# Optimization experiments

Hardware: AMD Instinct MI355X
Metric: run time of the kernel (lower is better)

Reference implementation:

```python
import jax, jax.numpy as jnp
import numpy as np

B, SQ, SK = 2, 2048, 2048   # batch, n_query, n_memory
D, H, DFF = 1024, 16, 1024  # model dim, heads, ffn dim (must equal D per source constraints)
DH = D // H                 # head dim = 64
NEG = 1e9


def _split_heads(x):
    # (B, S, D) -> (B, H, S, DH)
    b, s, _ = x.shape
    return x.reshape(b, s, H, DH).transpose(0, 2, 1, 3)


def setup_inputs() -> dict:
    key = jax.random.key(0)
    ks = jax.random.split(key, 10)
    s = 0.02
    return {
        "q": jax.random.normal(ks[0], (B, SQ, D), jnp.float32),
        "k": jax.random.normal(ks[1], (B, SK, D), jnp.float32),
        "v": jax.random.normal(ks[2], (B, SK, D), jnp.float32),
        "Win_w": jax.random.normal(ks[3], (DFF, D), jnp.float32) * s,
        "Win_b": jnp.zeros((DFF,), jnp.float32),
        "Wff_w": jax.random.normal(ks[4], (D, DFF), jnp.float32) * s,
        "Wff_b": jnp.zeros((D,), jnp.float32),
        "Wout_w": jax.random.normal(ks[5], (D, D), jnp.float32) * s,
        "Wout_b": jnp.zeros((D,), jnp.float32),
        "attn_mask": jax.random.randint(ks[6], (B, SK), 0, 2, jnp.int32),
    }


def reference(q, k, v, Win_w, Win_b, Wff_w, Wff_b, Wout_w, Wout_b, attn_mask):
    # projections (in_linear; k,v additionally pass through out_linear as in source)
    qh = q @ Win_w.T + Win_b
    kh = (k @ Win_w.T + Win_b) @ Wout_w.T + Wout_b
    vh = (v @ Win_w.T + Win_b) @ Wout_w.T + Wout_b
    qh = qh * (D ** -0.5)

    qh, kh, vh = _split_heads(qh), _split_heads(kh), _split_heads(vh)

    # additive mask bias: 0 where mask==1, -1e9 where mask==0, broadcast over heads/queries
    bias = (attn_mask.astype(jnp.float32) - 1.0) * NEG  # (B, SK)
    scores = jnp.einsum("bhqd,bhkd->bhqk", qh, kh) + bias[:, None, None, :]
    probs = jax.nn.softmax(scores, axis=-1)
    out = jnp.einsum("bhqk,bhkd->bhqd", probs, vh)

    # merge heads: (B, H, SQ, DH) -> (B, SQ, D)
    out = out.transpose(0, 2, 1, 3).reshape(B, SQ, D)

    out = out @ Wff_w.T + Wff_b
    out = out @ Wout_w.T + Wout_b
    return out
```

## Files before the change

### kernel.cpp

```cpp
#include <hip/hip_runtime.h>
#include <cstdint>
#include <cstddef>

using u16 = unsigned short;
using u32 = unsigned int;

typedef __attribute__((ext_vector_type(8))) short short8;
typedef __attribute__((ext_vector_type(4))) float f32x4;

#define MFMA16(a, b, c) __builtin_amdgcn_mfma_f32_16x16x32_bf16((a), (b), (c), 0, 0, 0)

#define QSCALE 0.0450842200f

__device__ __forceinline__ u16 f2bf(float f) {
  u32 u = __float_as_uint(f);
  return (u16)((u + 0x7FFFu + ((u >> 16) & 1u)) >> 16);
}

__device__ __forceinline__ u32 pack_bf16(float a, float b) {
  u32 r;
  asm("v_cvt_pk_bf16_f32 %0, %1, %2" : "=v"(r) : "v"(a), "v"(b));
  return r;
}

__device__ __forceinline__ void gload_lds16(const u16* g, u16* l) {
  __builtin_amdgcn_global_load_lds((const __attribute__((address_space(1))) void*)g,
                                   (__attribute__((address_space(3))) void*)l, 16, 0, 0);
}

__global__ __launch_bounds__(256) void prep_all(
    const float* __restrict__ q, const float* __restrict__ k, const float* __restrict__ v,
    const float* __restrict__ Wout_w, const float* __restrict__ Win_w,
    const float* __restrict__ Wff_w, const float* __restrict__ Win_b,
    const float* __restrict__ Wout_b, u16* __restrict__ X,
    u16* __restrict__ Woutb, u16* __restrict__ Winb,
    u16* __restrict__ WinT, u16* __restrict__ WffT,
    float* __restrict__ bias2, float* __restrict__ bias1f) {
  __shared__ float tile[64][68];
  const int t = threadIdx.x;
  const int bid = blockIdx.x;
  if (bid < 12288) {
    int i4 = bid * 256 + t;
    const float* src = (i4 < 1048576) ? q : (i4 < 2097152) ? k : v;
    int loc = i4 & 1048575;
    float4 w = reinterpret_cast<const float4*>(src)[loc];
    u32 lo = (u32)f2bf(w.x) | ((u32)f2bf(w.y) << 16);
    u32 hi = (u32)f2bf(w.z) | ((u32)f2bf(w.w) << 16);
    reinterpret_cast<uint2*>(X)[i4] = make_uint2(lo, hi);
  } else if (bid < 14336) {
    const int wb = bid - 12288;
    const float* src = wb < 1024 ? Wout_w : Win_w;
    u16* dst = wb < 1024 ? Woutb : Winb;
    const float sc = wb < 1024 ? 1.0f : QSCALE;
    int i = (wb & 1023) * 256 + t;
    float4 vv = reinterpret_cast<const float4*>(src)[i];
    u32 lo = (u32)f2bf(vv.x * sc) | ((u32)f2bf(vv.y * sc) << 16);
    u32 hi = (u32)f2bf(vv.z * sc) | ((u32)f2bf(vv.w * sc) << 16);
    reinterpret_cast<uint2*>(dst)[i] = make_uint2(lo, hi);
  } else if (bid < 14848) {
    const int tb = bid - 14336;
    const float* in = tb < 256 ? Win_w : Wff_w;
    u16* out = tb < 256 ? WinT : WffT;
    const int tix = tb & 255;
    const int bx = (tix >> 4) * 64, by = (tix & 15) * 64;
    const int r = t >> 2, c16 = (t & 3) * 16;
#pragma unroll
    for (int i = 0; i < 4; ++i)
      *reinterpret_cast<float4*>(&tile[r][c16 + i * 4]) =
          *reinterpret_cast<const float4*>(&in[(size_t)(bx + r) * 1024 + by + c16 + i * 4]);
    __syncthreads();
    const int jj = t >> 2, i16 = (t & 3) * 16;
#pragma unroll
    for (int i = 0; i < 4; ++i) {
      uint2 p;
      p.x = (u32)f2bf(tile[i16 + i * 4 + 0][jj]) | ((u32)f2bf(tile[i16 + i * 4 + 1][jj]) << 16);
      p.y = (u32)f2bf(tile[i16 + i * 4 + 2][jj]) | ((u32)f2bf(tile[i16 + i * 4 + 3][jj]) << 16);
      *reinterpret_cast<uint2*>(&out[(size_t)(by + jj) * 1024 + bx + i16 + i * 4]) = p;
    }
  } else if (bid < 15104) {
    const int w = t >> 6, l = t & 63;
    const int j = (bid - 14848) * 4 + w;
    const float4* Wr = reinterpret_cast<const float4*>(Wout_w + (size_t)j * 1024);
    const float4* br = reinterpret_cast<const float4*>(Win_b);
    float s = 0.f;
    for (int i = l; i < 256; i += 64) {
      float4 a = Wr[i], b = br[i];
      s += a.x * b.x + a.y * b.y + a.z * b.z + a.w * b.w;
    }
#pragma unroll
    for (int o = 1; o < 64; o <<= 1) s += __shfl_xor(s, o);
    if (l == 0) bias2[j] = s + Wout_b[j];
  } else {
    float4 vv = reinterpret_cast<const float4*>(Win_b)[t];
    vv.x *= QSCALE; vv.y *= QSCALE; vv.z *= QSCALE; vv.w *= QSCALE;
    reinterpret_cast<float4*>(bias1f)[t] = vv;
  }
}

__global__ __launch_bounds__(256) void gemm_w2(const u16* __restrict__ A,
                                               const u16* __restrict__ Bt0,
                                               const u16* __restrict__ Bt1,
                                               u16* __restrict__ C0,
                                               u16* __restrict__ C1) {
  const int bid = blockIdx.x;
  const int xcd = bid & 7, local = bid >> 3;
  const int z = local >> 5;
  const int mt = xcd * 2 + ((local >> 4) & 1);
  const int nt = local & 15;
  const u16* Bt = z ? Bt1 : Bt0;
  u16* C = z ? C1 : C0;
  __shared__ __align__(16) u16 As[2][4096];
  __shared__ __align__(16) u16 Bs[2][4096];
  const int t = threadIdx.x, w = t >> 6, l = t & 63;
  const int l15 = l & 15, l4 = l >> 4;
  const int m0 = mt * 64, n0 = nt * 64;
  f32x4 acc[4] = {};
  const int row0 = t >> 3, cs0 = t & 7;
  const int c0 = cs0 ^ (row0 & 7);
  const int row1 = row0 + 32;
  const int c1 = cs0 ^ (row1 & 7);
  const u16* gA0 = A + (size_t)(m0 + row0) * 1024 + c0 * 8;
  const u16* gA1 = A + (size_t)(m0 + row1) * 1024 + c1 * 8;
  const u16* gB0 = Bt + (size_t)(n0 + row0) * 1024 + c0 * 8;
  const u16* gB1 = Bt + (size_t)(n0 + row1) * 1024 + c1 * 8;
#define W2_STAGE(KK, DST)                             \
  gload_lds16(gA0 + (KK), &As[DST][0] + w * 512);     \
  gload_lds16(gA1 + (KK), &As[DST][2048] + w * 512);  \
  gload_lds16(gB0 + (KK), &Bs[DST][0] + w * 512);     \
  gload_lds16(gB1 + (KK), &Bs[DST][2048] + w * 512);
  W2_STAGE(0, 0)
  for (int step = 0; step < 16; ++step) {
    const int c = step & 1;
    __syncthreads();
    if (step < 15) { W2_STAGE((step + 1) * 64, c ^ 1) }
#pragma unroll
    for (int ks = 0; ks < 2; ++ks) {
      const int cc = ks * 4 + l4;
      short8 bfr = *reinterpret_cast<const short8*>(&Bs[c][(w * 16 + l15) * 64 + ((cc ^ (l15 & 7)) * 8)]);
#pragma unroll
      for (int i = 0; i < 4; ++i) {
        short8 afr = *reinterpret_cast<const short8*>(&As[c][(i * 16 + l15) * 64 + ((cc ^ (l15 & 7)) * 8)]);
        acc[i] = MFMA16(afr, bfr, acc[i]);
      }
    }
  }
#pragma unroll
  for (int i = 0; i < 4; ++i)
#pragma unroll
    for (int j = 0; j < 4; ++j)
      C[(size_t)(m0 + i * 16 + l4 * 4 + j) * 1024 + n0 + w * 16 + l15] = f2bf(acc[i][j]);
}

__global__ __launch_bounds__(256) void proj(const u16* __restrict__ X,
                                            const u16* __restrict__ Winb,
                                            const u16* __restrict__ Wc2,
                                            const float* __restrict__ bias1f,
                                            const float* __restrict__ bias2,
                                            u16* __restrict__ Qh,
                                            u16* __restrict__ Kp,
                                            u16* __restrict__ VT) {
  __shared__ __align__(16) u16 As[2][4096];
  __shared__ __align__(16) u16 Bs[2][4096];
  const int t = threadIdx.x, w = t >> 6, l = t & 63;
  const int l15 = l & 15, l4 = l >> 4;
  const int bid = blockIdx.x;
  const int xcd = bid & 7, local = bid >> 3;
  const int mt = xcd * 12 + (local >> 3);
  const int nt = local & 7;
  const int seg = mt >> 5;
  const int m0 = mt * 128;
  const int n0 = nt * 128;
  const int wr = (w >> 1) * 64, wc = (w & 1) * 64;
  const u16* Bt = seg == 0 ? Winb : Wc2;
  const float* bias = seg == 0 ? bias1f : bias2;

  f32x4 acc[4][4] = {};
  const int srow = t >> 2;
  const int sck = (t & 3) ^ ((t >> 3) & 3);
  const u16* gA = X + (size_t)(m0 + srow) * 1024 + sck * 8;
  const u16* gB = Bt + (size_t)(n0 + srow) * 1024 + sck * 8;
#define PJ_STAGE(KK, DST)                                   \
  gload_lds16(gA + (KK), &As[DST][0] + w * 512);            \
  gload_lds16(gA + (KK) + 65536, &As[DST][2048] + w * 512); \
  gload_lds16(gB + (KK), &Bs[DST][0] + w * 512);            \
  gload_lds16(gB + (KK) + 65536, &Bs[DST][2048] + w * 512);
  PJ_STAGE(0, 0)
  const int sw = (l15 >> 1) & 3;
  for (int step = 0; step < 32; ++step) {
    const int c = step & 1;
    __syncthreads();
    if (step < 31) { PJ_STAGE((step + 1) * 32, c ^ 1) }
    short8 af[4], bf[4];
#pragma unroll
    for (int i = 0; i < 4; ++i)
      af[i] = *reinterpret_cast<const short8*>(&As[c][(wr + i * 16 + l15) * 32 + ((l4 ^ sw) * 8)]);
#pragma unroll
    for (int i = 0; i < 4; ++i)
      bf[i] = *reinterpret_cast<const short8*>(&Bs[c][(wc + i * 16 + l15) * 32 + ((l4 ^ sw) * 8)]);
#pragma unroll
    for (int mi = 0; mi < 4; ++mi)
#pragma unroll
      for (int ni = 0; ni < 4; ++ni)
        acc[mi][ni] = MFMA16(af[mi], bf[ni], acc[mi][ni]);
  }

#pragma unroll
  for (int mi = 0; mi < 4; ++mi) {
#pragma unroll
    for (int ni = 0; ni < 4; ++ni) {
      const int col = n0 + wc + ni * 16 + l15;
      const float bv = bias[col];
      const int row0 = m0 + wr + mi * 16 + l4 * 4;
      if (seg == 0) {
#pragma unroll
        for (int j = 0; j < 4; ++j)
          Qh[(size_t)(row0 + j) * 1024 + col] = f2bf(acc[mi][ni][j] + bv);
      } else if (seg == 1) {
#pragma unroll
        for (int j = 0; j < 4; ++j)
          Kp[(size_t)(row0 - 4096 + j) * 1024 + col] = f2bf(acc[mi][ni][j] + bv);
      } else {
        const int r = row0 - 8192;
        const int bb = r >> 11;
        const int sk = r & 2047;
        u32 p0 = (u32)f2bf(acc[mi][ni][0] + bv) | ((u32)f2bf(acc[mi][ni][1] + bv) << 16);
        u32 p1 = (u32)f2bf(acc[mi][ni][2] + bv) | ((u32)f2bf(acc[mi][ni][3] + bv) << 16);
        *reinterpret_cast<uint2*>(VT + ((size_t)(bb * 1024 + col)) * 2048 + sk) = make_uint2(p0, p1);
      }
    }
  }
}

__global__ __launch_bounds__(256) void attn(const u16* __restrict__ Qh,
                                            const u16* __restrict__ Kb,
                                            const u16* __restrict__ VT,
                                            const int* __restrict__ mask,
                                            u16* __restrict__ AO,
                                            const float* __restrict__ Wout_w,
                                            const float* __restrict__ Wff_b,
                                            const float* __restrict__ Wout_b,
                                            float* __restrict__ bias3) {
  __shared__ __align__(16) u16 Kt[128 * 64];
  __shared__ __align__(16) u16 Vt[2][64 * 64];
  __shared__ float biasS[2048];
  const int t = threadIdx.x, l = t & 63, w = t >> 6;
  const int bid = blockIdx.x;

  if (bid >= 512) {
    const int j = (bid - 512) * 4 + w;
    const float4* Wr = reinterpret_cast<const float4*>(Wout_w + (size_t)j * 1024);
    const float4* br = reinterpret_cast<const float4*>(Wff_b);
    float s = 0.f;
    for (int i = l; i < 256; i += 64) {
      float4 a = Wr[i], b = br[i];
      s += a.x * b.x + a.y * b.y + a.z * b.z + a.w * b.w;
    }
#pragma unroll
    for (int o = 1; o < 64; o <<= 1) s += __shfl_xor(s, o);
    if (l == 0) bias3[j] = s + Wout_b[j];
    return;
  }

  const int l15 = l & 15, l4 = l >> 4;
  const int bh = (bid & 7) * 4 + ((bid >> 3) & 3);
  const int qb = bid >> 5;
  const int b = bh >> 4, h = bh & 15, q0 = qb * 128;

  for (int i = t; i < 2048; i += 256) biasS[i] = mask[b * 2048 + i] ? 0.f : -1.442695e9f;

  short8 qf[2][2];
#pragma unroll
  for (int qg = 0; qg < 2; ++qg) {
    const u16* qp =
        Qh + (size_t)(b * 2048 + q0 + w * 32 + qg * 16 + l15) * 1024 + h * 64 + l4 * 8;
    qf[qg][0] = *reinterpret_cast<const short8*>(qp);
    qf[qg][1] = *reinterpret_cast<const short8*>(qp + 32);
  }
  short8 ones;
#pragma unroll
  for (int i = 0; i < 8; ++i) ones[i] = (short)0x3F80;

  f32x4 acc[2][4] = {};
  f32x4 accS[2] = {};

  const int rr = t >> 3, cs = t & 7;
  const int ck = cs ^ (rr & 7);
  const int vb = (ck >> 2) * 32 + (ck & 3) * 4;
  const u16* gK = Kb + (size_t)(b * 2048 + rr) * 1024 + h * 64 + ck * 8;
  u16* ldsK = Kt + w * 512;
  const u32* gV0 = reinterpret_cast<const u32*>(VT) + (size_t)(b * 1024 + h * 64 + rr) * 1024;
  const u32* gV1 = gV0 + (size_t)32 * 1024;

  for (int kt = 0; kt < 2048; kt += 128) {
    const int ia = (kt >> 1) + (vb >> 1);
    uint2 a01 = *reinterpret_cast<const uint2*>(gV0 + ia);
    uint2 a89 = *reinterpret_cast<const uint2*>(gV0 + ia + 8);
    uint2 b01 = *reinterpret_cast<const uint2*>(gV0 + ia + 32);
    uint2 b89 = *reinterpret_cast<const uint2*>(gV0 + ia + 40);
    uint2 c01 = *reinterpret_cast<const uint2*>(gV1 + ia);
    uint2 c89 = *reinterpret_cast<const uint2*>(gV1 + ia + 8);
    uint2 d01 = *reinterpret_cast<const uint2*>(gV1 + ia + 32);
    uint2 d89 = *reinterpret_cast<const uint2*>(gV1 + ia + 40);
    __syncthreads();
    gload_lds16(gK + (size_t)kt * 1024, ldsK);
    gload_lds16(gK + (size_t)(kt + 32) * 1024, ldsK + 2048);
    gload_lds16(gK + (size_t)(kt + 64) * 1024, ldsK + 4096);
    gload_lds16(gK + (size_t)(kt + 96) * 1024, ldsK + 6144);
    *reinterpret_cast<uint4*>(&Vt[0][rr * 64 + cs * 8]) = make_uint4(a01.x, a01.y, a89.x, a89.y);
    *reinterpret_cast<uint4*>(&Vt[0][(rr + 32) * 64 + cs * 8]) =
        make_uint4(c01.x, c01.y, c89.x, c89.y);
    *reinterpret_cast<uint4*>(&Vt[1][rr * 64 + cs * 8]) = make_uint4(b01.x, b01.y, b89.x, b89.y);
    *reinterpret_cast<uint4*>(&Vt[1][(rr + 32) * 64 + cs * 8]) =
        make_uint4(d01.x, d01.y, d89.x, d89.y);
    __syncthreads();

#pragma unroll
    for (int half = 0; half < 2; ++half) {
      const int kb0 = kt + half * 64;
      f32x4 s[4][2];
#pragma unroll
      for (int n = 0; n < 4; ++n) {
        f32x4 bv4 = *reinterpret_cast<const f32x4*>(&biasS[kb0 + n * 16 + l4 * 4]);
        s[n][0] = bv4;
        s[n][1] = bv4;
      }
      __builtin_amdgcn_s_setprio(1);
#pragma unroll
      for (int ks = 0; ks < 2; ++ks) {
        const int cc = ks * 4 + l4;
#pragma unroll
        for (int n = 0; n < 4; ++n) {
          short8 kb = *reinterpret_cast<const short8*>(
              &Kt[(half * 64 + n * 16 + l15) * 64 + ((cc ^ (l15 & 7)) * 8)]);
          s[n][0] = MFMA16(kb, qf[0][ks], s[n][0]);
          s[n][1] = MFMA16(kb, qf[1][ks], s[n][1]);
        }
      }
      __builtin_amdgcn_s_setprio(0);
#pragma unroll
      for (int n = 0; n < 4; ++n)
#pragma unroll
        for (int qg = 0; qg < 2; ++qg)
#pragma unroll
          for (int j = 0; j < 4; ++j) s[n][qg][j] = __builtin_amdgcn_exp2f(s[n][qg][j]);
      short8 pa[2][2];
#pragma unroll
      for (int qg = 0; qg < 2; ++qg) {
        u32 paw[8];
        paw[0] = pack_bf16(s[0][qg][0], s[0][qg][1]);
        paw[1] = pack_bf16(s[0][qg][2], s[0][qg][3]);
        paw[2] = pack_bf16(s[1][qg][0], s[1][qg][1]);
        paw[3] = pack_bf16(s[1][qg][2], s[1][qg][3]);
        paw[4] = pack_bf16(s[2][qg][0], s[2][qg][1]);
        paw[5] = pack_bf16(s[2][qg][2], s[2][qg][3]);
        paw[6] = pack_bf16(s[3][qg][0], s[3][qg][1]);
        paw[7] = pack_bf16(s[3][qg][2], s[3][qg][3]);
        pa[qg][0] = *reinterpret_cast<const short8*>(&paw[0]);
        pa[qg][1] = *reinterpret_cast<const short8*>(&paw[4]);
      }
      __builtin_amdgcn_s_setprio(1);
#pragma unroll
      for (int ks = 0; ks < 2; ++ks) {
        const int cc = ks * 4 + l4;
#pragma unroll
        for (int n = 0; n < 4; ++n) {
          short8 vb8 = *reinterpret_cast<const short8*>(
              &Vt[half][(n * 16 + l15) * 64 + ((cc ^ (l15 & 7)) * 8)]);
          acc[0][n] = MFMA16(pa[0][ks], vb8, acc[0][n]);
          acc[1][n] = MFMA16(pa[1][ks], vb8, acc[1][n]);
        }
        accS[0] = MFMA16(pa[0][ks], ones, accS[0]);
        accS[1] = MFMA16(pa[1][ks], ones, accS[1]);
      }
      __builtin_amdgcn_s_setprio(0);
    }
  }

#pragma unroll
  for (int qg = 0; qg < 2; ++qg) {
    const size_t orow0 = (size_t)(b * 2048 + q0 + w * 32 + qg * 16 + l4 * 4);
#pragma unroll
    for (int j = 0; j < 4; ++j) {
      const float inv = 1.0f / accS[qg][j];
#pragma unroll
      for (int n = 0; n < 4; ++n)
        AO[(orow0 + j) * 1024 + h * 64 + n * 16 + l15] = f2bf(acc[qg][n][j] * inv);
    }
  }
}

__global__ __launch_bounds__(256) void gemm_tail(const u16* __restrict__ A,
                                                 const u16* __restrict__ Bt,
                                                 const float* __restrict__ bias,
                                                 float* __restrict__ C) {
  __shared__ __align__(16) u16 As[2][4096];
  __shared__ __align__(16) u16 Bs[2][2048];
  const int t = threadIdx.x, w = t >> 6, l = t & 63;
  const int l15 = l & 15, l4 = l >> 4;
  const int bid = blockIdx.x;
  const int xcd = bid & 7, local = bid >> 3;
  const int mt = xcd * 4 + (local >> 4);
  const int nt = local & 15;
  const int m0 = mt * 128, n0 = nt * 64;
  const int wr = (w >> 1) * 64, wc = (w & 1) * 32;
  f32x4 acc[4][2] = {};
  const int srow = t >> 2;
  const int sck = (t & 3) ^ ((t >> 3) & 3);
  const u16* gA = A + (size_t)(m0 + srow) * 1024 + sck * 8;
  const u16* gB = Bt + (size_t)(n0 + srow) * 1024 + sck * 8;
#define TL_STAGE(KK, DST)                                   \
  gload_lds16(gA + (KK), &As[DST][0] + w * 512);            \
  gload_lds16(gA + (KK) + 65536, &As[DST][2048] + w * 512); \
  gload_lds16(gB + (KK), &Bs[DST][0] + w * 512);
  TL_STAGE(0, 0)
  const int sw = (l15 >> 1) & 3;
  for (int step = 0; step < 32; ++step) {
    const int c = step & 1;
    __syncthreads();
    if (step < 31) { TL_STAGE((step + 1) * 32, c ^ 1) }
    short8 af[4], bf[2];
#pragma unroll
    for (int i = 0; i < 4; ++i)
      af[i] = *reinterpret_cast<const short8*>(&As[c][(wr + i * 16 + l15) * 32 + ((l4 ^ sw) * 8)]);
#pragma unroll
    for (int i = 0; i < 2; ++i)
      bf[i] = *reinterpret_cast<const short8*>(&Bs[c][(wc + i * 16 + l15) * 32 + ((l4 ^ sw) * 8)]);
#pragma unroll
    for (int mi = 0; mi < 4; ++mi)
#pragma unroll
      for (int ni = 0; ni < 2; ++ni)
        acc[mi][ni] = MFMA16(af[mi], bf[ni], acc[mi][ni]);
  }
#pragma unroll
  for (int mi = 0; mi < 4; ++mi) {
#pragma unroll
    for (int ni = 0; ni < 2; ++ni) {
      const int col = n0 + wc + ni * 16 + l15;
      const float bv = bias[col];
      const int row0 = m0 + wr + mi * 16 + l4 * 4;
#pragma unroll
      for (int j = 0; j < 4; ++j)
        C[(size_t)(row0 + j) * 1024 + col] = acc[mi][ni][j] + bv;
    }
  }
}

extern "C" void kernel_launch(void* const* d_in, const int* in_sizes, int n_in,
                              void* d_out, int out_size, void* d_ws, size_t ws_size,
                              hipStream_t stream) {
  const float* q = (const float*)d_in[0];
  const float* k = (const float*)d_in[1];
  const float* v = (const float*)d_in[2];
  const float* Win_w = (const float*)d_in[3];
  const float* Win_b = (const float*)d_in[4];
  const float* Wff_w = (const float*)d_in[5];
  const float* Wff_b = (const float*)d_in[6];
  const float* Wout_w = (const float*)d_in[7];
  const float* Wout_b = (const float*)d_in[8];
  const int* mask = (const int*)d_in[9];
  float* out = (float*)d_out;

  char* ws = (char*)d_ws;
  u16* Xbf = (u16*)ws;
  u16* AO = (u16*)ws;
  float* bias3 = (float*)(ws + 20971520);
  u16* Qh = (u16*)(ws + 25165824);
  u16* WinT = (u16*)(ws + 25165824);
  u16* Woutb = (u16*)(ws + 27262976);
  u16* WffT = (u16*)(ws + 29360128);
  u16* Kproj = (u16*)(ws + 33554432);
  u16* VT = (u16*)(ws + 41943040);
  u16* Wc2 = (u16*)(ws + 50331648);
  u16* Wc3 = (u16*)(ws + 52428800);
  u16* Winb = (u16*)(ws + 54525952);
  float* bias2 = out;
  float* bias1f = out + 1024;

  prep_all<<<15105, 256, 0, stream>>>(q, k, v, Wout_w, Win_w, Wff_w, Win_b, Wout_b,
                                      Xbf, Woutb, Winb, WinT, WffT, bias2, bias1f);
  gemm_w2<<<512, 256, 0, stream>>>(Woutb, WinT, WffT, Wc2, Wc3);
  proj<<<768, 256, 0, stream>>>(Xbf, Winb, Wc2, bias1f, bias2, Qh, Kproj, VT);
  attn<<<768, 256, 0, stream>>>(Qh, Kproj, VT, mask, AO, Wout_w, Wff_b, Wout_b, bias3);
  gemm_tail<<<512, 256, 0, stream>>>(AO, Wc3, bias3, out);
}
```

Before: 144.9 us.

## Split attention over two key halves and merge partials in a separate kernel

The attention kernel now runs over half of the key sequence per block, which doubles the attention grid from 512 to 1024 blocks. Each block writes unnormalized bf16 partial outputs and per-row softmax denominators. A new merge kernel adds the two partials and divides by the summed denominators. The small bias3 reduction moves from the attention kernel into the merge kernel. This targets under-occupancy of the GPU in attention, at the cost of an extra launch, extra partial-output memory traffic, and a second bf16 rounding of the partial sums. The split relies on no per-half max subtraction being needed, which the unnormalized exp accumulation already assumes.

```diff
diff --git a/kernel.cpp b/kernel.cpp
--- a/kernel.cpp
+++ b/kernel.cpp
@@ -15,6 +15,10 @@
 __device__ __forceinline__ u16 f2bf(float f) {
   u32 u = __float_as_uint(f);
   return (u16)((u + 0x7FFFu + ((u >> 16) & 1u)) >> 16);
+}
+
+__device__ __forceinline__ float bf2f(u32 lo16) {
+  return __uint_as_float(lo16 << 16);
 }
 
 __device__ __forceinline__ u32 pack_bf16(float a, float b) {
@@ -235,38 +239,21 @@
                                             const u16* __restrict__ Kb,
                                             const u16* __restrict__ VT,
                                             const int* __restrict__ mask,
-                                            u16* __restrict__ AO,
-                                            const float* __restrict__ Wout_w,
-                                            const float* __restrict__ Wff_b,
-                                            const float* __restrict__ Wout_b,
-                                            float* __restrict__ bias3) {
+                                            u16* __restrict__ PP,
+                                            float* __restrict__ S_part) {
   __shared__ __align__(16) u16 Kt[128 * 64];
   __shared__ __align__(16) u16 Vt[2][64 * 64];
-  __shared__ float biasS[2048];
+  __shared__ float biasS[1024];
   const int t = threadIdx.x, l = t & 63, w = t >> 6;
   const int bid = blockIdx.x;
-
-  if (bid >= 512) {
-    const int j = (bid - 512) * 4 + w;
-    const float4* Wr = reinterpret_cast<const float4*>(Wout_w + (size_t)j * 1024);
-    const float4* br = reinterpret_cast<const float4*>(Wff_b);
-    float s = 0.f;
-    for (int i = l; i < 256; i += 64) {
-      float4 a = Wr[i], b = br[i];
-      s += a.x * b.x + a.y * b.y + a.z * b.z + a.w * b.w;
-    }
-#pragma unroll
-    for (int o = 1; o < 64; o <<= 1) s += __shfl_xor(s, o);
-    if (l == 0) bias3[j] = s + Wout_b[j];
-    return;
-  }
-
   const int l15 = l & 15, l4 = l >> 4;
   const int bh = (bid & 7) * 4 + ((bid >> 3) & 3);
-  const int qb = bid >> 5;
+  const int rest = bid >> 5;
+  const int qb = rest & 15, kh = rest >> 4;
   const int b = bh >> 4, h = bh & 15, q0 = qb * 128;
-
-  for (int i = t; i < 2048; i += 256) biasS[i] = mask[b * 2048 + i] ? 0.f : -1.442695e9f;
+  const int k0g = kh * 1024;
+
+  for (int i = t; i < 1024; i += 256) biasS[i] = mask[b * 2048 + k0g + i] ? 0.f : -1.442695e9f;
 
   short8 qf[2][2];
 #pragma unroll
@@ -286,13 +273,13 @@
   const int rr = t >> 3, cs = t & 7;
   const int ck = cs ^ (rr & 7);
   const int vb = (ck >> 2) * 32 + (ck & 3) * 4;
-  const u16* gK = Kb + (size_t)(b * 2048 + rr) * 1024 + h * 64 + ck * 8;
+  const u16* gK = Kb + (size_t)(b * 2048 + k0g + rr) * 1024 + h * 64 + ck * 8;
   u16* ldsK = Kt + w * 512;
   const u32* gV0 = reinterpret_cast<const u32*>(VT) + (size_t)(b * 1024 + h * 64 + rr) * 1024;
   const u32* gV1 = gV0 + (size_t)32 * 1024;
 
-  for (int kt = 0; kt < 2048; kt += 128) {
-    const int ia = (kt >> 1) + (vb >> 1);
+  for (int kt = 0; kt < 1024; kt += 128) {
+    const int ia = ((k0g + kt) >> 1) + (vb >> 1);
     uint2 a01 = *reinterpret_cast<const uint2*>(gV0 + ia);
     uint2 a89 = *reinterpret_cast<const uint2*>(gV0 + ia + 8);
     uint2 b01 = *reinterpret_cast<const uint2*>(gV0 + ia + 32);
@@ -376,16 +363,59 @@
     }
   }
 
+  u16* PPk = PP + (size_t)kh * 4194304;
 #pragma unroll
   for (int qg = 0; qg < 2; ++qg) {
     const size_t orow0 = (size_t)(b * 2048 + q0 + w * 32 + qg * 16 + l4 * 4);
 #pragma unroll
-    for (int j = 0; j < 4; ++j) {
-      const float inv = 1.0f / accS[qg][j];
+    for (int j = 0; j < 4; ++j)
 #pragma unroll
       for (int n = 0; n < 4; ++n)
-        AO[(orow0 + j) * 1024 + h * 64 + n * 16 + l15] = f2bf(acc[qg][n][j] * inv);
-    }
+        PPk[(orow0 + j) * 1024 + h * 64 + n * 16 + l15] = f2bf(acc[qg][n][j]);
+    if (l15 == 0) {
+#pragma unroll
+      for (int j = 0; j < 4; ++j) S_part[kh * 4096 + orow0 + j] = accS[qg][j];
+    }
+  }
+}
+
+__global__ __launch_bounds__(256) void attn_merge(const u16* __restrict__ PP,
+                                                  const float* __restrict__ S_part,
+                                                  const float* __restrict__ Wout_w,
+                                                  const float* __restrict__ Wff_b,
+                                                  const float* __restrict__ Wout_b,
+                                                  u16* __restrict__ AO,
+                                                  float* __restrict__ bias3) {
+  const int bid = blockIdx.x, t = threadIdx.x;
+  if (bid < 2048) {
+    const size_t e8 = ((size_t)bid * 256 + t) * 8;
+    const int row = (int)(e8 >> 10);
+    const float inv = 1.0f / (S_part[row] + S_part[4096 + row]);
+    uint4 a = *reinterpret_cast<const uint4*>(PP + e8);
+    uint4 c = *reinterpret_cast<const uint4*>(PP + 4194304 + e8);
+    u32 aw[4] = {a.x, a.y, a.z, a.w};
+    u32 cw[4] = {c.x, c.y, c.z, c.w};
+    u32 r[4];
+#pragma unroll
+    for (int i = 0; i < 4; ++i) {
+      float f0 = (bf2f(aw[i] & 0xffffu) + bf2f(cw[i] & 0xffffu)) * inv;
+      float f1 = (bf2f(aw[i] >> 16) + bf2f(cw[i] >> 16)) * inv;
+      r[i] = pack_bf16(f0, f1);
+    }
+    *reinterpret_cast<uint4*>(AO + e8) = make_uint4(r[0], r[1], r[2], r[3]);
+  } else {
+    const int w = t >> 6, l = t & 63;
+    const int j = (bid - 2048) * 4 + w;
+    const float4* Wr = reinterpret_cast<const float4*>(Wout_w + (size_t)j * 1024);
+    const float4* br = reinterpret_cast<const float4*>(Wff_b);
+    float s = 0.f;
+    for (int i = l; i < 256; i += 64) {
+      float4 a = Wr[i], b = br[i];
+      s += a.x * b.x + a.y * b.y + a.z * b.z + a.w * b.w;
+    }
+#pragma unroll
+    for (int o = 1; o < 64; o <<= 1) s += __shfl_xor(s, o);
+    if (l == 0) bias3[j] = s + Wout_b[j];
   }
 }
 
@@ -463,9 +493,10 @@
   char* ws = (char*)d_ws;
   u16* Xbf = (u16*)ws;
   u16* AO = (u16*)ws;
-  float* bias3 = (float*)(ws + 20971520);
+  u16* PP = (u16*)(ws + 8388608);
   u16* Qh = (u16*)(ws + 25165824);
   u16* WinT = (u16*)(ws + 25165824);
+  float* bias3 = (float*)(ws + 25165824);
   u16* Woutb = (u16*)(ws + 27262976);
   u16* WffT = (u16*)(ws + 29360128);
   u16* Kproj = (u16*)(ws + 33554432);
@@ -475,11 +506,13 @@
   u16* Winb = (u16*)(ws + 54525952);
   float* bias2 = out;
   float* bias1f = out + 1024;
+  float* S_part = out + 4096;
 
   prep_all<<<15105, 256, 0, stream>>>(q, k, v, Wout_w, Win_w, Wff_w, Win_b, Wout_b,
                                       Xbf, Woutb, Winb, WinT, WffT, bias2, bias1f);
   gemm_w2<<<512, 256, 0, stream>>>(Woutb, WinT, WffT, Wc2, Wc3);
   proj<<<768, 256, 0, stream>>>(Xbf, Winb, Wc2, bias1f, bias2, Qh, Kproj, VT);
-  attn<<<768, 256, 0, stream>>>(Qh, Kproj, VT, mask, AO, Wout_w, Wff_b, Wout_b, bias3);
+  attn<<<1024, 256, 0, stream>>>(Qh, Kproj, VT, mask, PP, S_part);
+  attn_merge<<<2304, 256, 0, stream>>>(PP, S_part, Wout_w, Wff_b, Wout_b, AO, bias3);
   gemm_tail<<<512, 256, 0, stream>>>(AO, Wc3, bias3, out);
 }
```

Measured after the change: 153.3 us. +5.8%, slower.
